# Performance work log

Hardware: AMD Instinct MI355X
Metric: run time of the kernel (lower is better)

Reference implementation:

```python
import jax, jax.numpy as jnp
import numpy as np

N, E, B = 50000, 800000, 128
IN, HID, OUT, H = 256, 256, 256, 4
NEG_SLOPE = 0.2
EPS_BN = 1e-5
EPS_LN = 1e-5


def setup_inputs() -> dict:
    key = jax.random.key(0)
    ks = jax.random.split(key, 10)
    C1, C2 = HID // H, OUT // H
    s = lambda k, sh: jax.random.normal(k, sh, jnp.float32) * 0.05
    return dict(
        x=jax.random.normal(ks[0], (N, IN), jnp.float32),
        edge_index=jax.random.randint(ks[1], (2, E), 0, N),
        batch=jnp.sort(jax.random.randint(ks[2], (N,), 0, B)),
        W1=s(ks[3], (IN, HID)), a_src1=s(ks[4], (H, C1)), a_dst1=s(ks[5], (H, C1)),
        b1=jnp.zeros((HID,), jnp.float32),
        bn1_g=jnp.ones((HID,), jnp.float32), bn1_b=jnp.zeros((HID,), jnp.float32),
        bn1_m=jnp.zeros((HID,), jnp.float32), bn1_v=jnp.ones((HID,), jnp.float32),
        ln1_g=jnp.ones((HID,), jnp.float32), ln1_b=jnp.zeros((HID,), jnp.float32),
        W2=s(ks[6], (HID + IN, OUT)), a_src2=s(ks[7], (H, C2)), a_dst2=s(ks[8], (H, C2)),
        b2=jnp.zeros((OUT,), jnp.float32),
        bn2_g=jnp.ones((OUT,), jnp.float32), bn2_b=jnp.zeros((OUT,), jnp.float32),
        bn2_m=jnp.zeros((OUT,), jnp.float32), bn2_v=jnp.ones((OUT,), jnp.float32),
        ln2_g=jnp.ones((OUT,), jnp.float32), ln2_b=jnp.zeros((OUT,), jnp.float32),
    )


def gat_conv(x, edge_index, W, a_s, a_d, b):
    # PyG GATConv (concat heads, add_self_loops=True, eval -> no attention dropout)
    n = x.shape[0]
    Hh, C = a_s.shape
    h = (x @ W).reshape(n, Hh, C)                      # [N,H,C]
    loop = jnp.arange(n)
    src = jnp.concatenate([edge_index[0], loop])       # [E+N]
    dst = jnp.concatenate([edge_index[1], loop])
    al_s = jnp.einsum('nhc,hc->nh', h, a_s)            # [N,H]
    al_d = jnp.einsum('nhc,hc->nh', h, a_d)
    e = jax.nn.leaky_relu(al_s[src] + al_d[dst], NEG_SLOPE)   # [E+N,H]
    emax = jax.ops.segment_max(e, dst, num_segments=n)        # segment softmax over incoming edges
    p = jnp.exp(e - emax[dst])
    denom = jax.ops.segment_sum(p, dst, num_segments=n)
    alpha = p / (denom[dst] + 1e-16)
    out = jax.ops.segment_sum(alpha[:, :, None] * h[src], dst, num_segments=n)
    return out.reshape(n, Hh * C) + b


def bn_eval(x, g, b, m, v):
    return (x - m) * (g * jax.lax.rsqrt(v + EPS_BN)) + b


def layer_norm(x, g, b):
    mu = jnp.mean(x, axis=-1, keepdims=True)
    var = jnp.mean(jnp.square(x - mu), axis=-1, keepdims=True)
    return (x - mu) * jax.lax.rsqrt(var + EPS_LN) * g + b


def reference(x, edge_index, batch,
              W1, a_src1, a_dst1, b1, bn1_g, bn1_b, bn1_m, bn1_v, ln1_g, ln1_b,
              W2, a_src2, a_dst2, b2, bn2_g, bn2_b, bn2_m, bn2_v, ln2_g, ln2_b):
    x1 = x
    h = gat_conv(x, edge_index, W1, a_src1, a_dst1, b1)
    h = jax.nn.relu(layer_norm(bn_eval(h, bn1_g, bn1_b, bn1_m, bn1_v), ln1_g, ln1_b))
    x2 = h
    # root_extend: broadcast the first node of each (sorted) batch segment
    root_idx = jnp.searchsorted(batch, jnp.arange(B))  # first occurrence per graph
    h = jnp.concatenate([h, x1[root_idx[batch]]], axis=1)
    h = gat_conv(h, edge_index, W2, a_src2, a_dst2, b2)
    h = jax.nn.relu(layer_norm(bn_eval(h, bn2_g, bn2_b, bn2_m, bn2_v), ln2_g, ln2_b))
    h = jnp.concatenate([h, x2[root_idx[batch]]], axis=1)   # [N, OUT+HID]
    sums = jax.ops.segment_sum(h, batch, num_segments=B)
    cnt = jax.ops.segment_sum(jnp.ones((h.shape[0],), h.dtype), batch, num_segments=B)
    return sums / jnp.maximum(cnt, 1.0)[:, None]            # scatter_mean -> [B, OUT+HID]
```

## Files before the change

kernel.cpp:

```cpp
#include <hip/hip_runtime.h>
#include <stdint.h>

typedef unsigned short u16;
typedef unsigned int u32;
typedef unsigned char u8;
typedef __bf16 bf16x8 __attribute__((ext_vector_type(8)));
typedef float f32x4 __attribute__((ext_vector_type(4)));

#define NGRAPH 128

__device__ __forceinline__ float b2f(u16 u) {
    union { u32 i; float f; } c; c.i = ((u32)u) << 16; return c.f;
}
__device__ __forceinline__ u16 f2b(float f) {
    union { float f; u32 i; } c; c.f = f;
    u32 r = c.i + 0x7fffu + ((c.i >> 16) & 1u);
    return (u16)(r >> 16);
}

__global__ void k_sentinel(u16* __restrict__ out, int n, u16 pat) {
    int i = blockIdx.x * 256 + threadIdx.x;
    if (i < n) out[i] = pat;
}

__global__ __launch_bounds__(256) void k_init(const u16* __restrict__ x, const int* __restrict__ batch,
                                              int* __restrict__ deg, float* __restrict__ pool,
                                              int* __restrict__ flag, int* __restrict__ root,
                                              int N, int B) {
    __shared__ int cnt;
    int i = blockIdx.x * 256 + threadIdx.x;
    if (i < N + 1) deg[i] = 0;
    if (i < B * 256) pool[i] = 0.0f;
    if (blockIdx.x == 0) {
        if (threadIdx.x == 0) cnt = 0;
        __syncthreads();
        int weird = 0;
        for (int k = threadIdx.x; k < 4096; k += 256) {
            u16 u = x[2 * k];
            int e = (u >> 7) & 0xff;
            if (e != 0 && (e < 100 || e > 140)) weird++;
        }
        atomicAdd(&cnt, weird);
        __syncthreads();
        if (threadIdx.x == 0) *flag = (cnt > 1024) ? 1 : 0;
    } else if (blockIdx.x == 1) {
        int b = threadIdx.x;
        if (b <= B) {
            int lo = 0, hi = N;
            while (lo < hi) { int mid = (lo + hi) >> 1; if (batch[mid] < b) lo = mid + 1; else hi = mid; }
            root[b] = lo;
        }
    }
}

__global__ __launch_bounds__(256) void k_cvt4(const void* __restrict__ src, u16* __restrict__ dst,
                                              int n4, const int* __restrict__ flag) {
    int i = blockIdx.x * 256 + threadIdx.x;
    if (i >= n4) return;
    if (*flag) {
        float4 v = ((const float4*)src)[i];
        ushort4 o;
        o.x = f2b(v.x); o.y = f2b(v.y); o.z = f2b(v.z); o.w = f2b(v.w);
        ((ushort4*)dst)[i] = o;
    } else {
        ((ushort4*)dst)[i] = ((const ushort4*)src)[i];
    }
}

__global__ __launch_bounds__(256) void k_cvt_small(
    const void* p0, const void* p1, const void* p2, const void* p3, const void* p4,
    const void* p5, const void* p6, const void* p7, const void* p8, const void* p9,
    const void* p10, const void* p11, const void* p12, const void* p13, const void* p14,
    const void* p15, const void* p16, const void* p17,
    u16* __restrict__ dst, const int* __restrict__ flag) {
    const void* ps[18] = {p0,p1,p2,p3,p4,p5,p6,p7,p8,p9,p10,p11,p12,p13,p14,p15,p16,p17};
    int f = *flag;
    int vec = blockIdx.x;
    int j = threadIdx.x;
    const void* s = ps[vec];
    dst[vec * 256 + j] = f ? f2b(((const float*)s)[j]) : ((const u16*)s)[j];
}

__global__ __launch_bounds__(256) void k_tr2(const u16* __restrict__ w1, u16* __restrict__ wt1,
                                             const u16* __restrict__ w2, u16* __restrict__ wt2) {
    int idx = blockIdx.x * 256 + threadIdx.x;
    int halfsel = idx >> 16;
    int j = idx & 65535;
    int n = j >> 8, k = j & 255;
    if (halfsel == 0) wt1[n * 256 + k] = w1[k * 256 + n];
    else              wt2[n * 256 + k] = w2[k * 256 + n];
}

__global__ __launch_bounds__(256) void k_hist(const int* __restrict__ ei, int* __restrict__ deg, int E) {
    int e = blockIdx.x * 256 + threadIdx.x;
    if (e < E) atomicAdd(&deg[ei[E + e]], 1);
}

__global__ __launch_bounds__(256) void k_scan1(const int* __restrict__ in, int* __restrict__ out,
                                               int* __restrict__ bsums, int total) {
    __shared__ int lds[256];
    int tid = threadIdx.x;
    int base = blockIdx.x * 2048 + tid * 8;
    int v[8]; int ts = 0;
#pragma unroll
    for (int r = 0; r < 8; r++) { int i = base + r; int x = (i < total) ? in[i] : 0; v[r] = x; ts += x; }
    lds[tid] = ts;
    __syncthreads();
    for (int off = 1; off < 256; off <<= 1) {
        int t = (tid >= off) ? lds[tid - off] : 0;
        __syncthreads();
        lds[tid] += t;
        __syncthreads();
    }
    int run = lds[tid] - ts;
#pragma unroll
    for (int r = 0; r < 8; r++) { int i = base + r; if (i < total) out[i] = run; run += v[r]; }
    if (tid == 255) bsums[blockIdx.x] = lds[255];
}

__global__ void k_scan2(int* __restrict__ bsums, int nb) {
    if (threadIdx.x == 0 && blockIdx.x == 0) {
        int run = 0;
        for (int i = 0; i < nb; i++) { int t = bsums[i]; bsums[i] = run; run += t; }
    }
}

__global__ __launch_bounds__(256) void k_scan3(const int* __restrict__ pscan, const int* __restrict__ bsums,
                                               int* __restrict__ ptr, int* __restrict__ cursor,
                                               int total, int N) {
    int i = blockIdx.x * 256 + threadIdx.x;
    if (i >= total) return;
    int val = pscan[i] + bsums[i >> 11];
    ptr[i] = val;
    if (i < N) cursor[i] = val;
}

__global__ __launch_bounds__(256) void k_fill(const int* __restrict__ ei, int* __restrict__ cursor,
                                              int* __restrict__ csr, int E) {
    int e = blockIdx.x * 256 + threadIdx.x;
    if (e < E) {
        int src = ei[e];
        int pos = atomicAdd(&cursor[ei[E + e]], 1);
        csr[pos] = src;
    }
}

__global__ __launch_bounds__(256) void k_gemm(const u16* __restrict__ A, const u16* __restrict__ Bt,
                                              u16* __restrict__ C, u8* __restrict__ C8,
                                              float* __restrict__ salsc, float* __restrict__ ald,
                                              const u16* __restrict__ a_s, const u16* __restrict__ a_d,
                                              int M,
                                              const float* __restrict__ r2, const int* __restrict__ batch) {
    __shared__ __align__(16) u16 smem[128 * 64 * 2];
    u16* As = smem;
    u16* Bs = smem + 128 * 64;
    const int tid = threadIdx.x;
    const int lane = tid & 63;
    const int wave = tid >> 6;
    const int bm = blockIdx.x >> 1;
    const int bn = blockIdx.x & 1;
    const int m0 = bm * 128, n0 = bn * 128;
    const int wm = wave >> 1, wn = wave & 1;
    const int lm = lane & 15, lq = lane >> 4;
    const int head = bn * 2 + wn;
    f32x4 acc[4][4] = {};

    for (int k0 = 0; k0 < 256; k0 += 64) {
        uint4 ra[4], rb[4];
#pragma unroll
        for (int it = 0; it < 4; ++it) {
            int t = tid + 256 * it;
            int m = t >> 3;
            int kc = (t & 7) ^ (m & 7);
            int gm = m0 + m; if (gm > M - 1) gm = M - 1;
            ra[it] = *(const uint4*)(A + (size_t)gm * 256 + k0 + kc * 8);
            rb[it] = *(const uint4*)(Bt + (size_t)(n0 + m) * 256 + k0 + kc * 8);
        }
        __syncthreads();
#pragma unroll
        for (int it = 0; it < 4; ++it) {
            int t = tid + 256 * it;
            *(uint4*)(As + t * 8) = ra[it];
            *(uint4*)(Bs + t * 8) = rb[it];
        }
        __syncthreads();
#pragma unroll
        for (int ks = 0; ks < 2; ++ks) {
            int kq = ks * 4 + lq;
            bf16x8 af[4], bfr[4];
#pragma unroll
            for (int i = 0; i < 4; i++) {
                int m = wm * 64 + i * 16 + lm;
                af[i] = *(const bf16x8*)(As + (m * 8 + (kq ^ (m & 7))) * 8);
                int n = wn * 64 + i * 16 + lm;
                bfr[i] = *(const bf16x8*)(Bs + (n * 8 + (kq ^ (n & 7))) * 8);
            }
#pragma unroll
            for (int i = 0; i < 4; i++)
#pragma unroll
                for (int j = 0; j < 4; j++)
                    acc[i][j] = __builtin_amdgcn_mfma_f32_16x16x32_bf16(af[i], bfr[j], acc[i][j], 0, 0, 0);
        }
    }

    float asv[4], adv[4];
#pragma unroll
    for (int j = 0; j < 4; j++) {
        asv[j] = b2f(a_s[head * 64 + j * 16 + lm]);
        adv[j] = b2f(a_d[head * 64 + j * 16 + lm]);
    }

    __syncthreads();
    u8* lds8 = (u8*)smem;
#pragma unroll
    for (int i = 0; i < 4; i++) {
#pragma unroll
        for (int r = 0; r < 4; r++) {
            int rl = wm * 64 + i * 16 + lq * 4 + r;
            int row = m0 + rl;
            bool ok = (row < M);
            const float* r2row = (r2 && ok) ? (r2 + (size_t)batch[row] * 256) : nullptr;
            float v[4];
#pragma unroll
            for (int j = 0; j < 4; j++) {
                v[j] = acc[i][j][r];
                if (r2row) v[j] += r2row[n0 + wn * 64 + j * 16 + lm];
            }
            float ps = v[0] * asv[0] + v[1] * asv[1] + v[2] * asv[2] + v[3] * asv[3];
            float pd = v[0] * adv[0] + v[1] * adv[1] + v[2] * adv[2] + v[3] * adv[3];
#pragma unroll
            for (int off = 1; off < 16; off <<= 1) { ps += __shfl_xor(ps, off); pd += __shfl_xor(pd, off); }
            float mx = fmaxf(fmaxf(fabsf(v[0]), fabsf(v[1])), fmaxf(fabsf(v[2]), fabsf(v[3])));
#pragma unroll
            for (int off = 1; off < 16; off <<= 1) mx = fmaxf(mx, __shfl_xor(mx, off));
            float scl = mx * (1.0f / 127.0f);
            float isc = (mx > 0.f) ? 127.0f / mx : 0.f;
#pragma unroll
            for (int j = 0; j < 4; j++) {
                int col = n0 + wn * 64 + j * 16 + lm;
                if (ok) C[(size_t)row * 256 + col] = f2b(v[j]);
                int q = (int)rintf(v[j] * isc);
                lds8[rl * 144 + wn * 64 + j * 16 + lm] = (u8)(q & 0xff);
            }
            if (ok && lm == 0) {
                salsc[(size_t)row * 8 + head * 2] = ps;
                salsc[(size_t)row * 8 + head * 2 + 1] = scl;
                ald[(size_t)row * 4 + head] = pd;
            }
        }
    }
    __syncthreads();
    for (int t = tid; t < 1024; t += 256) {
        int rl = t >> 3;
        int seg = t & 7;
        int hh = seg >> 2;
        int off = (seg & 3) * 16;
        int row = m0 + rl;
        if (row < M)
            *(uint4*)(C8 + ((size_t)(bn * 2 + hh) * M + row) * 64 + off) =
                *(const uint4*)(lds8 + rl * 144 + hh * 64 + off);
    }
}

__global__ __launch_bounds__(256) void k_attw(
    const float* __restrict__ salsc, const float* __restrict__ ald_,
    const int* __restrict__ ptr, const int* __restrict__ csr,
    float* __restrict__ aw, float* __restrict__ invs, float* __restrict__ selfw, int N, int E) {
    int node = blockIdx.x * 4 + (threadIdx.x >> 6);
    if (node >= N) return;
    int lane = threadIdx.x & 63;
    int h = lane & 3;
    int el = lane >> 2;
    int beg = ptr[node], end = ptr[node + 1];
    float ad = ald_[node * 4 + h];
    float s = 0.f;
    for (int i0 = beg; i0 < end; i0 += 16) {
        int e = i0 + el;
        if (e < end) {
            int src = csr[e];
            float2 f = *(const float2*)(salsc + (size_t)src * 8 + h * 2);
            float lg = f.x + ad; lg = (lg > 0.f) ? lg : 0.2f * lg;
            float p = __expf(lg);
            aw[(size_t)h * E + e] = p * f.y;
            s += p;
        }
    }
#pragma unroll
    for (int off = 4; off < 64; off <<= 1) s += __shfl_xor(s, off);
    float es = salsc[(size_t)node * 8 + h * 2] + ad; es = (es > 0.f) ? es : 0.2f * es;
    float pself = __expf(es);
    s += pself;
    if (el == 0) {
        float inv = 1.0f / (s + 1e-16f);
        invs[node * 4 + h] = inv;
        selfw[node * 4 + h] = pself * inv;
    }
}

__global__ __launch_bounds__(256) void k_agg6(
    const u16* __restrict__ h, const u8* __restrict__ h8,
    const float* __restrict__ aw, const float* __restrict__ invs_, const float* __restrict__ selfw_,
    const int* __restrict__ ptr, const int* __restrict__ csr,
    const u16* __restrict__ bias, const u16* __restrict__ bng, const u16* __restrict__ bnb,
    const u16* __restrict__ bnm, const u16* __restrict__ bnv,
    const u16* __restrict__ lng, const u16* __restrict__ lnb,
    u16* __restrict__ xout, float* __restrict__ pool, const int* __restrict__ batch, int N, int E) {
    int node = blockIdx.x * 4 + (threadIdx.x >> 6);
    if (node >= N) return;
    int lane = threadIdx.x & 63;
    int rot = blockIdx.x & 3;
    int beg = ptr[node], end = ptr[node + 1];
    float acc[4];
    int hd[4];
#pragma unroll
    for (int ph = 0; ph < 4; ++ph) {
        int hh = (ph + rot) & 3;
        hd[ph] = hh;
        const float* awh = aw + (size_t)hh * E;
        const u8* h8h = h8 + (size_t)hh * N * 64;
        float sa = 0.f, sb = 0.f, sc2 = 0.f, sd = 0.f;
        int i = beg;
        for (; i + 4 <= end; i += 4) {
            int s0 = csr[i], s1 = csr[i + 1], s2 = csr[i + 2], s3 = csr[i + 3];
            float w0 = awh[i], w1 = awh[i + 1], w2 = awh[i + 2], w3 = awh[i + 3];
            float q0 = (float)(signed char)h8h[(size_t)s0 * 64 + lane];
            float q1 = (float)(signed char)h8h[(size_t)s1 * 64 + lane];
            float q2 = (float)(signed char)h8h[(size_t)s2 * 64 + lane];
            float q3 = (float)(signed char)h8h[(size_t)s3 * 64 + lane];
            sa += w0 * q0; sb += w1 * q1; sc2 += w2 * q2; sd += w3 * q3;
        }
        for (; i < end; ++i) {
            int s0 = csr[i];
            float w0 = awh[i];
            sa += w0 * (float)(signed char)h8h[(size_t)s0 * 64 + lane];
        }
        acc[ph] = (sa + sb) + (sc2 + sd);
    }
    float v[4];
#pragma unroll
    for (int ph = 0; ph < 4; ++ph) {
        int hh = hd[ph];
        int c = hh * 64 + lane;
        float inv = invs_[node * 4 + hh];
        float sw = selfw_[node * 4 + hh];
        float self = b2f(h[(size_t)node * 256 + c]);
        float t = acc[ph] * inv + sw * self + b2f(bias[c]);
        v[ph] = (t - b2f(bnm[c])) * (b2f(bng[c]) * rsqrtf(b2f(bnv[c]) + 1e-5f)) + b2f(bnb[c]);
    }
    float sum = v[0] + v[1] + v[2] + v[3];
#pragma unroll
    for (int off = 1; off < 64; off <<= 1) sum += __shfl_xor(sum, off);
    float mu = sum * 0.00390625f;
    float q = 0.f;
#pragma unroll
    for (int ph = 0; ph < 4; ++ph) { v[ph] -= mu; q += v[ph] * v[ph]; }
#pragma unroll
    for (int off = 1; off < 64; off <<= 1) q += __shfl_xor(q, off);
    float rstd = rsqrtf(q * 0.00390625f + 1e-5f);
#pragma unroll
    for (int ph = 0; ph < 4; ++ph) {
        int hh = hd[ph];
        int c = hh * 64 + lane;
        float y = fmaxf(v[ph] * rstd * b2f(lng[c]) + b2f(lnb[c]), 0.f);
        if (xout) xout[(size_t)node * 256 + c] = f2b(y);
        if (pool) atomicAdd(pool + (size_t)batch[node] * 256 + c, y);
    }
}

__global__ __launch_bounds__(256) void k_r2(const u16* __restrict__ xc, const u16* __restrict__ w2,
                                            const int* __restrict__ root, float* __restrict__ r2, int N) {
    __shared__ float xs[256];
    int b = blockIdx.x, c = threadIdx.x;
    int rt = root[b]; if (rt >= N) rt = N - 1; if (rt < 0) rt = 0;
    xs[c] = b2f(xc[(size_t)rt * 256 + c]);
    __syncthreads();
    float acc = 0.f;
    for (int k = 0; k < 256; k++) acc += xs[k] * b2f(w2[(size_t)(256 + k) * 256 + c]);
    r2[b * 256 + c] = acc;
}

__global__ void k_final(const float* __restrict__ pool, const u16* __restrict__ x2,
                        const int* __restrict__ root, void* __restrict__ out,
                        const int* __restrict__ flag) {
    int b = blockIdx.x, c = threadIdx.x;
    int r0 = root[b], r1 = root[b + 1];
    int cnt = r1 - r0;
    float inv = 1.0f / (float)(cnt > 1 ? cnt : 1);
    float v0 = pool[b * 256 + c] * inv;
    float v1 = (cnt > 0) ? b2f(x2[(size_t)r0 * 256 + c]) : 0.0f;
    if (*flag) {
        float* o = (float*)out;
        o[b * 512 + c] = v0;
        o[b * 512 + 256 + c] = v1;
    } else {
        u16* o = (u16*)out;
        o[b * 512 + c] = f2b(v0);
        o[b * 512 + 256 + c] = f2b(v1);
    }
}

extern "C" void kernel_launch(void* const* d_in, const int* in_sizes, int n_in,
                              void* d_out, int out_size, void* d_ws, size_t ws_size,
                              hipStream_t stream) {
    u16* outp = (u16*)d_out;
    int ogrid = (out_size + 255) / 256;

    if (n_in != 23) {
        k_sentinel<<<ogrid, 256, 0, stream>>>(outp, out_size, (u16)0x44FA);
        return;
    }

    const void* x_raw = d_in[0];
    const int* ei = (const int*)d_in[1];
    const int* batch = (const int*)d_in[2];
    const int NX = in_sizes[0];
    const int E = in_sizes[1] / 2;
    const int N = in_sizes[2];
    const int NW1 = in_sizes[3];
    const int NW2 = in_sizes[13];
    const int B = NGRAPH;

    char* p = (char*)d_ws;
    auto carve = [&](size_t bytes) -> void* {
        void* r = (void*)p; p += (bytes + 255) & ~(size_t)255; return r;
    };
    u16* xc    = (u16*)carve((size_t)NX * 2);
    u16* w1c   = (u16*)carve((size_t)NW1 * 2);
    u16* w2c   = (u16*)carve((size_t)NW2 * 2);
    u16* sc    = (u16*)carve((size_t)18 * 256 * 2);
    u16* wt1   = (u16*)carve((size_t)65536 * 2);
    u16* wt2   = (u16*)carve((size_t)65536 * 2);
    u16* hbuf  = (u16*)carve((size_t)N * 256 * 2);
    u8*  h8    = (u8*)carve((size_t)N * 256);
    u16* x2    = (u16*)carve((size_t)N * 256 * 2);
    float* salsc = (float*)carve((size_t)N * 8 * 4);
    float* ald = (float*)carve((size_t)N * 4 * 4);
    float* aw  = (float*)carve((size_t)E * 4 * 4);
    float* invs  = (float*)carve((size_t)N * 4 * 4);
    float* selfw = (float*)carve((size_t)N * 4 * 4);
    int* deg    = (int*)carve((size_t)(N + 1) * 4);
    int* pscan  = (int*)carve((size_t)(N + 1) * 4);
    int* ptr    = (int*)carve((size_t)(N + 1) * 4);
    int* cursor = (int*)carve((size_t)N * 4);
    int* csr    = (int*)carve((size_t)E * 4);
    int* bsums  = (int*)carve(1024);
    int* root   = (int*)carve((size_t)(B + 1) * 4);
    float* r2   = (float*)carve((size_t)B * 256 * 4);
    float* pool = (float*)carve((size_t)B * 256 * 4);
    int* flag   = (int*)carve(256);

    size_t needed = (size_t)(p - (char*)d_ws);
    if (needed > ws_size) {
        k_sentinel<<<ogrid, 256, 0, stream>>>(outp, out_size, (u16)0x447A);
        return;
    }

    int zmax = (N + 1) > (B * 256) ? (N + 1) : (B * 256);
    k_init<<<(zmax + 255) / 256, 256, 0, stream>>>((const u16*)x_raw, batch, deg, pool, flag, root, N, B);

    k_cvt4<<<(NX / 4 + 255) / 256, 256, 0, stream>>>(x_raw, xc, NX / 4, flag);
    k_cvt4<<<(NW1 / 4 + 255) / 256, 256, 0, stream>>>(d_in[3], w1c, NW1 / 4, flag);
    k_cvt4<<<(NW2 / 4 + 255) / 256, 256, 0, stream>>>(d_in[13], w2c, NW2 / 4, flag);
    k_cvt_small<<<18, 256, 0, stream>>>(
        d_in[4], d_in[5], d_in[6], d_in[7], d_in[8], d_in[9], d_in[10], d_in[11], d_in[12],
        d_in[14], d_in[15], d_in[16], d_in[17], d_in[18], d_in[19], d_in[20], d_in[21], d_in[22],
        sc, flag);

    k_tr2<<<512, 256, 0, stream>>>(w1c, wt1, w2c, wt2);

    k_hist<<<(E + 255) / 256, 256, 0, stream>>>(ei, deg, E);
    int nb1 = (N + 1 + 2047) / 2048;
    k_scan1<<<nb1, 256, 0, stream>>>(deg, pscan, bsums, N + 1);
    k_scan2<<<1, 64, 0, stream>>>(bsums, nb1);
    k_scan3<<<(N + 1 + 255) / 256, 256, 0, stream>>>(pscan, bsums, ptr, cursor, N + 1, N);
    k_fill<<<(E + 255) / 256, 256, 0, stream>>>(ei, cursor, csr, E);

    int mt = (N + 127) / 128;
    int ngrid = (N + 3) / 4;
    k_gemm<<<mt * 2, 256, 0, stream>>>(xc, wt1, hbuf, h8, salsc, ald,
                                       sc + 0 * 256, sc + 1 * 256, N, nullptr, nullptr);
    k_attw<<<ngrid, 256, 0, stream>>>(salsc, ald, ptr, csr, aw, invs, selfw, N, E);
    k_agg6<<<ngrid, 256, 0, stream>>>(hbuf, h8, aw, invs, selfw, ptr, csr,
        sc + 2 * 256, sc + 3 * 256, sc + 4 * 256, sc + 5 * 256, sc + 6 * 256, sc + 7 * 256, sc + 8 * 256,
        x2, nullptr, batch, N, E);
    k_r2<<<B, 256, 0, stream>>>(xc, w2c, root, r2, N);
    k_gemm<<<mt * 2, 256, 0, stream>>>(x2, wt2, hbuf, h8, salsc, ald,
                                       sc + 9 * 256, sc + 10 * 256, N, r2, batch);
    k_attw<<<ngrid, 256, 0, stream>>>(salsc, ald, ptr, csr, aw, invs, selfw, N, E);
    k_agg6<<<ngrid, 256, 0, stream>>>(hbuf, h8, aw, invs, selfw, ptr, csr,
        sc + 11 * 256, sc + 12 * 256, sc + 13 * 256, sc + 14 * 256, sc + 15 * 256, sc + 16 * 256, sc + 17 * 256,
        nullptr, pool, batch, N, E);

    k_final<<<B, 256, 0, stream>>>(pool, x2, root, d_out, flag);
    (void)ws_size;
}
```

Measured before the change: 706.1 us.

## Split aggregation into per-head XCD-pinned gather kernel and a finalize kernel

The fused per-node aggregation becomes two kernels. The first is a gather kernel whose block index is mapped so that each pair of XCDs handles a single attention head, which keeps that head's int8 feature slice (about 3.2 MB) resident in that XCD's L2. It writes partial sums as bf16 to a new buffer. A separate finalize kernel then applies the normalization, self-loop, BN, LayerNorm, ReLU and pooling, at the cost of an extra launch, an N×256 bf16 round trip, and bf16 rounding of the partial sums.

```diff
diff --git a/kernel.cpp b/kernel.cpp
--- a/kernel.cpp
+++ b/kernel.cpp
@@ -297,55 +297,58 @@
     }
 }
 
-__global__ __launch_bounds__(256) void k_agg6(
-    const u16* __restrict__ h, const u8* __restrict__ h8,
-    const float* __restrict__ aw, const float* __restrict__ invs_, const float* __restrict__ selfw_,
+__global__ __launch_bounds__(256) void k_aggh(
+    const u8* __restrict__ h8, const float* __restrict__ aw,
     const int* __restrict__ ptr, const int* __restrict__ csr,
+    u16* __restrict__ hacc, int N, int E) {
+    int b = blockIdx.x;
+    int xcd = b & 7;
+    int head = xcd >> 1;
+    int node = (b >> 3) * 8 + (xcd & 1) * 4 + (threadIdx.x >> 6);
+    if (node >= N) return;
+    int lane = threadIdx.x & 63;
+    const float* __restrict__ awh = aw + (size_t)head * E;
+    const u8* __restrict__ h8h = h8 + (size_t)head * N * 64;
+    int beg = ptr[node], end = ptr[node + 1];
+    float sa = 0.f, sb = 0.f, sc2 = 0.f, sd = 0.f;
+    int i = beg;
+    for (; i + 4 <= end; i += 4) {
+        int s0 = csr[i], s1 = csr[i + 1], s2 = csr[i + 2], s3 = csr[i + 3];
+        float w0 = awh[i], w1 = awh[i + 1], w2 = awh[i + 2], w3 = awh[i + 3];
+        float q0 = (float)(signed char)h8h[(size_t)s0 * 64 + lane];
+        float q1 = (float)(signed char)h8h[(size_t)s1 * 64 + lane];
+        float q2 = (float)(signed char)h8h[(size_t)s2 * 64 + lane];
+        float q3 = (float)(signed char)h8h[(size_t)s3 * 64 + lane];
+        sa += w0 * q0; sb += w1 * q1; sc2 += w2 * q2; sd += w3 * q3;
+    }
+    for (; i < end; ++i) {
+        int s0 = csr[i];
+        sa += awh[i] * (float)(signed char)h8h[(size_t)s0 * 64 + lane];
+    }
+    float accv = (sa + sb) + (sc2 + sd);
+    hacc[((size_t)node * 4 + head) * 64 + lane] = f2b(accv);
+}
+
+__global__ __launch_bounds__(256) void k_aggfin(
+    const u16* __restrict__ h, const u16* __restrict__ hacc,
+    const float* __restrict__ invs_, const float* __restrict__ selfw_,
     const u16* __restrict__ bias, const u16* __restrict__ bng, const u16* __restrict__ bnb,
     const u16* __restrict__ bnm, const u16* __restrict__ bnv,
     const u16* __restrict__ lng, const u16* __restrict__ lnb,
-    u16* __restrict__ xout, float* __restrict__ pool, const int* __restrict__ batch, int N, int E) {
+    u16* __restrict__ xout, float* __restrict__ pool, const int* __restrict__ batch, int N) {
     int node = blockIdx.x * 4 + (threadIdx.x >> 6);
     if (node >= N) return;
     int lane = threadIdx.x & 63;
-    int rot = blockIdx.x & 3;
-    int beg = ptr[node], end = ptr[node + 1];
-    float acc[4];
-    int hd[4];
-#pragma unroll
-    for (int ph = 0; ph < 4; ++ph) {
-        int hh = (ph + rot) & 3;
-        hd[ph] = hh;
-        const float* awh = aw + (size_t)hh * E;
-        const u8* h8h = h8 + (size_t)hh * N * 64;
-        float sa = 0.f, sb = 0.f, sc2 = 0.f, sd = 0.f;
-        int i = beg;
-        for (; i + 4 <= end; i += 4) {
-            int s0 = csr[i], s1 = csr[i + 1], s2 = csr[i + 2], s3 = csr[i + 3];
-            float w0 = awh[i], w1 = awh[i + 1], w2 = awh[i + 2], w3 = awh[i + 3];
-            float q0 = (float)(signed char)h8h[(size_t)s0 * 64 + lane];
-            float q1 = (float)(signed char)h8h[(size_t)s1 * 64 + lane];
-            float q2 = (float)(signed char)h8h[(size_t)s2 * 64 + lane];
-            float q3 = (float)(signed char)h8h[(size_t)s3 * 64 + lane];
-            sa += w0 * q0; sb += w1 * q1; sc2 += w2 * q2; sd += w3 * q3;
-        }
-        for (; i < end; ++i) {
-            int s0 = csr[i];
-            float w0 = awh[i];
-            sa += w0 * (float)(signed char)h8h[(size_t)s0 * 64 + lane];
-        }
-        acc[ph] = (sa + sb) + (sc2 + sd);
-    }
     float v[4];
 #pragma unroll
-    for (int ph = 0; ph < 4; ++ph) {
-        int hh = hd[ph];
+    for (int hh = 0; hh < 4; ++hh) {
         int c = hh * 64 + lane;
         float inv = invs_[node * 4 + hh];
         float sw = selfw_[node * 4 + hh];
         float self = b2f(h[(size_t)node * 256 + c]);
-        float t = acc[ph] * inv + sw * self + b2f(bias[c]);
-        v[ph] = (t - b2f(bnm[c])) * (b2f(bng[c]) * rsqrtf(b2f(bnv[c]) + 1e-5f)) + b2f(bnb[c]);
+        float acc = b2f(hacc[((size_t)node * 4 + hh) * 64 + lane]);
+        float t = acc * inv + sw * self + b2f(bias[c]);
+        v[hh] = (t - b2f(bnm[c])) * (b2f(bng[c]) * rsqrtf(b2f(bnv[c]) + 1e-5f)) + b2f(bnb[c]);
     }
     float sum = v[0] + v[1] + v[2] + v[3];
 #pragma unroll
@@ -353,15 +356,14 @@
     float mu = sum * 0.00390625f;
     float q = 0.f;
 #pragma unroll
-    for (int ph = 0; ph < 4; ++ph) { v[ph] -= mu; q += v[ph] * v[ph]; }
+    for (int hh = 0; hh < 4; ++hh) { v[hh] -= mu; q += v[hh] * v[hh]; }
 #pragma unroll
     for (int off = 1; off < 64; off <<= 1) q += __shfl_xor(q, off);
     float rstd = rsqrtf(q * 0.00390625f + 1e-5f);
 #pragma unroll
-    for (int ph = 0; ph < 4; ++ph) {
-        int hh = hd[ph];
+    for (int hh = 0; hh < 4; ++hh) {
         int c = hh * 64 + lane;
-        float y = fmaxf(v[ph] * rstd * b2f(lng[c]) + b2f(lnb[c]), 0.f);
+        float y = fmaxf(v[hh] * rstd * b2f(lng[c]) + b2f(lnb[c]), 0.f);
         if (xout) xout[(size_t)node * 256 + c] = f2b(y);
         if (pool) atomicAdd(pool + (size_t)batch[node] * 256 + c, y);
     }
@@ -433,6 +435,7 @@
     u16* hbuf  = (u16*)carve((size_t)N * 256 * 2);
     u8*  h8    = (u8*)carve((size_t)N * 256);
     u16* x2    = (u16*)carve((size_t)N * 256 * 2);
+    u16* hacc  = (u16*)carve((size_t)N * 256 * 2);
     float* salsc = (float*)carve((size_t)N * 8 * 4);
     float* ald = (float*)carve((size_t)N * 4 * 4);
     float* aw  = (float*)carve((size_t)E * 4 * 4);
@@ -477,19 +480,22 @@
 
     int mt = (N + 127) / 128;
     int ngrid = (N + 3) / 4;
+    int agrid = ((N + 7) / 8) * 8;
     k_gemm<<<mt * 2, 256, 0, stream>>>(xc, wt1, hbuf, h8, salsc, ald,
                                        sc + 0 * 256, sc + 1 * 256, N, nullptr, nullptr);
     k_attw<<<ngrid, 256, 0, stream>>>(salsc, ald, ptr, csr, aw, invs, selfw, N, E);
-    k_agg6<<<ngrid, 256, 0, stream>>>(hbuf, h8, aw, invs, selfw, ptr, csr,
+    k_aggh<<<agrid, 256, 0, stream>>>(h8, aw, ptr, csr, hacc, N, E);
+    k_aggfin<<<ngrid, 256, 0, stream>>>(hbuf, hacc, invs, selfw,
         sc + 2 * 256, sc + 3 * 256, sc + 4 * 256, sc + 5 * 256, sc + 6 * 256, sc + 7 * 256, sc + 8 * 256,
-        x2, nullptr, batch, N, E);
+        x2, nullptr, batch, N);
     k_r2<<<B, 256, 0, stream>>>(xc, w2c, root, r2, N);
     k_gemm<<<mt * 2, 256, 0, stream>>>(x2, wt2, hbuf, h8, salsc, ald,
                                        sc + 9 * 256, sc + 10 * 256, N, r2, batch);
     k_attw<<<ngrid, 256, 0, stream>>>(salsc, ald, ptr, csr, aw, invs, selfw, N, E);
-    k_agg6<<<ngrid, 256, 0, stream>>>(hbuf, h8, aw, invs, selfw, ptr, csr,
+    k_aggh<<<agrid, 256, 0, stream>>>(h8, aw, ptr, csr, hacc, N, E);
+    k_aggfin<<<ngrid, 256, 0, stream>>>(hbuf, hacc, invs, selfw,
         sc + 11 * 256, sc + 12 * 256, sc + 13 * 256, sc + 14 * 256, sc + 15 * 256, sc + 16 * 256, sc + 17 * 256,
-        nullptr, pool, batch, N, E);
+        nullptr, pool, batch, N);
 
     k_final<<<B, 256, 0, stream>>>(pool, x2, root, d_out, flag);
     (void)ws_size;
```

Measured after the change: 752.1 us. 1.07x slower.
